# Kernel optimization log

Hardware: AMD Instinct MI355X
Metric: run time of the kernel (lower is better)

The kernel has to match this reference:

```python
import jax, jax.numpy as jnp
import numpy as np

B, N, IN_DIM, D, H, L = 4, 2048, 1, 256, 8, 4
DH = D // H          # 32 head dim
ROPE_D = DH // 2     # 16 = rotary dim per spatial axis (relative_emb_dim=2)
MIN_FREQ_SCALE = 64.0  # scale / min_freq = 1.0 / (1/64)
EPS = 1e-5


def setup_inputs():
    key = jax.random.key(0)
    ks = jax.random.split(key, 12)
    s = 0.02
    return {
        'h': jax.random.normal(ks[0], (B, N, IN_DIM), jnp.float32),
        'pos': jax.random.uniform(ks[1], (B, N, 2), jnp.float32),
        'proj_w': jax.random.normal(ks[2], (IN_DIM, D), jnp.float32) * s,
        'proj_b': jnp.zeros((D,), jnp.float32),
        'qkv_w': jax.random.normal(ks[3], (L, D, 3 * D), jnp.float32) * s,
        'out_w': jax.random.normal(ks[4], (L, D, D), jnp.float32) * s,
        'out_b': jnp.zeros((L, D), jnp.float32),
        'O_w': jax.random.normal(ks[5], (L, D, D), jnp.float32) * s,
        'O_b': jnp.zeros((L, D), jnp.float32),
        'ffn1_w': jax.random.normal(ks[6], (L, D, 2 * D), jnp.float32) * s,
        'ffn1_b': jnp.zeros((L, 2 * D), jnp.float32),
        'ffn2_w': jax.random.normal(ks[7], (L, 2 * D, D), jnp.float32) * s,
        'ffn2_b': jnp.zeros((L, D), jnp.float32),
        'ln1_g': jnp.ones((L, D), jnp.float32),
        'ln1_b': jnp.zeros((L, D), jnp.float32),
        'ln2_g': jnp.ones((L, D), jnp.float32),
        'ln2_b': jnp.zeros((L, D), jnp.float32),
        'final_w': jax.random.normal(ks[8], (D, D), jnp.float32) * s,
    }


def _rope_freqs(coords):
    # coords: (B, N) -> freqs (B, N, ROPE_D)
    inv_freq = 1.0 / (10000.0 ** (jnp.arange(0, ROPE_D, 2, dtype=jnp.float32) / ROPE_D))
    f = (coords * MIN_FREQ_SCALE)[..., None] * inv_freq
    return jnp.concatenate([f, f], axis=-1)


def _rotate_half(x):
    d = x.shape[-1] // 2
    return jnp.concatenate([-x[..., d:], x[..., :d]], axis=-1)


def _apply_rope(t, f):
    return t * jnp.cos(f) + _rotate_half(t) * jnp.sin(f)


def _apply_2d_rope(t, ft, fx):
    d = t.shape[-1] // 2
    return jnp.concatenate([_apply_rope(t[..., :d], ft), _apply_rope(t[..., d:], fx)], axis=-1)


def _ln(x, g, b):
    m = jnp.mean(x, -1, keepdims=True)
    v = jnp.mean((x - m) ** 2, -1, keepdims=True)
    return (x - m) / jnp.sqrt(v + EPS) * g + b


def _forward(h, pos, proj_w, proj_b, qkv_w, out_w, out_b, O_w, O_b,
             ffn1_w, ffn1_b, ffn2_w, ffn2_b, ln1_g, ln1_b, ln2_g, ln2_b, final_w):
    h = h @ proj_w + proj_b                      # (B, N, D)
    ft = _rope_freqs(pos[..., 0])[:, None]       # (B, 1, N, ROPE_D) broadcast over heads
    fx = _rope_freqs(pos[..., 1])[:, None]
    scale = DH ** -0.5
    for l in range(L):
        qkv = h @ qkv_w[l]                       # (B, N, 3D)
        q, k, v = jnp.split(qkv, 3, axis=-1)
        to_heads = lambda t: t.reshape(B, N, H, DH).transpose(0, 2, 1, 3)
        q, k, v = to_heads(q), to_heads(k), to_heads(v)
        q = _apply_2d_rope(q, ft, fx)
        k = _apply_2d_rope(k, ft, fx)
        attn = jax.nn.softmax(jnp.einsum('bhid,bhjd->bhij', q, k) * scale, axis=-1)
        o = jnp.einsum('bhij,bhjd->bhid', attn, v)
        o = o.transpose(0, 2, 1, 3).reshape(B, N, D)
        o = o @ out_w[l] + out_b[l]              # attention to_out
        o = o @ O_w[l] + O_b[l]                  # layer O projection
        h = _ln(h + o, ln1_g[l], ln1_b[l])
        f = jax.nn.relu(h @ ffn1_w[l] + ffn1_b[l]) @ ffn2_w[l] + ffn2_b[l]
        h = _ln(h + f, ln2_g[l], ln2_b[l])
    return h @ final_w


def reference(h, pos, proj_w, proj_b, qkv_w, out_w, out_b, O_w, O_b,
              ffn1_w, ffn1_b, ffn2_w, ffn2_b, ln1_g, ln1_b, ln2_g, ln2_b, final_w):
    return _forward(h, pos, proj_w, proj_b, qkv_w, out_w, out_b, O_w, O_b,
                    ffn1_w, ffn1_b, ffn2_w, ffn2_b, ln1_g, ln1_b, ln2_g, ln2_b, final_w)
```

## Files before the change

kernel.cpp:

```cpp
#include <hip/hip_runtime.h>
#include <math.h>

#define B_ 4
#define N_ 2048
#define D_ 256
#define H_ 8
#define L_ 4
#define DH_ 32

typedef float f32x4 __attribute__((ext_vector_type(4)));
typedef short short8 __attribute__((ext_vector_type(8)));
typedef unsigned short ushort_t;
typedef ushort_t ushortx4 __attribute__((ext_vector_type(4)));
typedef ushort_t ushortx8 __attribute__((ext_vector_type(8)));

static __device__ __forceinline__ ushort_t f2bf(float x) {
    unsigned int u = __float_as_uint(x);
    unsigned int r = (u + 0x7fffu + ((u >> 16) & 1u)) >> 16;
    return (ushort_t)r;
}

static __device__ __forceinline__ unsigned int cvt_pk_bf16(float a, float b) {
    unsigned int w;
    asm("v_cvt_pk_bf16_f32 %0, %1, %2" : "=v"(w) : "v"(a), "v"(b));
    return w;
}

__global__ __launch_bounds__(256) void proj_kernel(
    const float* __restrict__ hin, const float* __restrict__ w,
    const float* __restrict__ bias, float* __restrict__ hout,
    ushort_t* __restrict__ hb)
{
    long idx = (long)blockIdx.x * 256 + threadIdx.x;
    long bn = idx >> 6;
    int d4 = (int)(idx & 63) << 2;
    float hv = hin[bn];
    float4 wv = *(const float4*)&w[d4];
    float4 bv = *(const float4*)&bias[d4];
    float4 o;
    o.x = hv * wv.x + bv.x;
    o.y = hv * wv.y + bv.y;
    o.z = hv * wv.z + bv.z;
    o.w = hv * wv.w + bv.w;
    *(float4*)&hout[bn * D_ + d4] = o;
    ushortx4 ob;
    ob[0] = f2bf(o.x); ob[1] = f2bf(o.y); ob[2] = f2bf(o.z); ob[3] = f2bf(o.w);
    *(ushortx4*)&hb[bn * D_ + d4] = ob;
}

__global__ __launch_bounds__(256) void rope_table_kernel(
    const float* __restrict__ pos, float* __restrict__ tab)
{
    int i = blockIdx.x * 256 + threadIdx.x;
    if (i >= B_ * N_) return;
    float t = pos[i * 2 + 0] * 64.0f;
    float x = pos[i * 2 + 1] * 64.0f;
    float* o = tab + (long)i * 32;
    const float log2_1e4_over8 = 13.28771237954945f / 8.0f;
    #pragma unroll
    for (int j = 0; j < 8; ++j) {
        float invf = exp2f(-(float)j * log2_1e4_over8);
        float st, ct, sx, cx;
        sincosf(t * invf, &st, &ct);
        sincosf(x * invf, &sx, &cx);
        o[j]      = ct;
        o[8 + j]  = st;
        o[16 + j] = cx;
        o[24 + j] = sx;
    }
}

__global__ __launch_bounds__(256) void rope_convert_kernel(
    const float* __restrict__ qkv, const float* __restrict__ tab,
    ushort_t* __restrict__ Qb, ushort_t* __restrict__ Kb)
{
    const float F = 0.17677669529663687f * 1.4426950408889634f;
    long idx = (long)blockIdx.x * 256 + threadIdx.x;
    int p = (int)(idx & 15);
    int h = (int)((idx >> 4) & 7);
    long bn = idx >> 7;
    int half = p >> 3;
    int j = p & 7;
    const float* tb = tab + bn * 32;
    float c = tb[half * 16 + j];
    float s = tb[half * 16 + 8 + j];
    float cF = c * F, sF = s * F;
    int b = (int)(bn >> 11);
    int n = (int)(bn & 2047);
    long obase = ((long)(b * H_ + h) * N_ + n) * DH_;
    const float* base = qkv + bn * (3 * D_) + h * DH_ + half * 16 + j;
    int d0 = half * 16 + j;
    float q0 = base[0], q1 = base[8];
    Qb[obase + d0]     = f2bf(q0 * cF - q1 * sF);
    Qb[obase + d0 + 8] = f2bf(q1 * cF + q0 * sF);
    float k0 = base[D_], k1 = base[D_ + 8];
    Kb[obase + d0]     = f2bf(k0 * c - k1 * s);
    Kb[obase + d0 + 8] = f2bf(k1 * c + k0 * s);
}

__global__ __launch_bounds__(256) void vtrans_kernel(
    const float* __restrict__ qkv, ushort_t* __restrict__ Vt)
{
    int bh = blockIdx.y;
    int b = bh >> 3, h = bh & 7;
    int n0 = blockIdx.x << 6;
    __shared__ float T[64][36];
    int t = threadIdx.x;
    int r = t >> 2, c0 = (t & 3) << 3;
    const float* src = qkv + ((long)b * N_ + n0 + r) * (3 * D_) + 2 * D_ + h * DH_ + c0;
    float4 a = ((const float4*)src)[0];
    float4 bb = ((const float4*)src)[1];
    *(float4*)&T[r][c0] = a;
    *(float4*)&T[r][c0 + 4] = bb;
    __syncthreads();
    int d = t >> 3, n8 = (t & 7) << 3;
    ushortx8 o;
    #pragma unroll
    for (int i = 0; i < 8; ++i) o[i] = f2bf(T[n8 + i][d]);
    *(ushortx8*)&Vt[((long)bh * DH_ + d) * N_ + n0 + n8] = o;
}

__global__ __launch_bounds__(256) void wprep_kernel(
    const float* __restrict__ qkv_w, const float* __restrict__ out_w,
    const float* __restrict__ O_w, const float* __restrict__ ffn1_w,
    const float* __restrict__ ffn2_w, const float* __restrict__ final_w,
    ushort_t* __restrict__ WT)
{
    int bid = blockIdx.x;
    const float* src; ushort_t* dst; int K, Nn, tile;
    if (bid < 192)      { int l = bid / 48;        tile = bid % 48;        src = qkv_w  + (long)l * 196608; dst = WT + (long)l * 196608;           K = 256; Nn = 768; }
    else if (bid < 256) { int r = bid - 192; int l = r / 16; tile = r % 16; src = out_w  + (long)l * 65536;  dst = WT + 786432  + (long)l * 65536;  K = 256; Nn = 256; }
    else if (bid < 320) { int r = bid - 256; int l = r / 16; tile = r % 16; src = O_w    + (long)l * 65536;  dst = WT + 1048576 + (long)l * 65536;  K = 256; Nn = 256; }
    else if (bid < 448) { int r = bid - 320; int l = r / 32; tile = r % 32; src = ffn1_w + (long)l * 131072; dst = WT + 1310720 + (long)l * 131072; K = 256; Nn = 512; }
    else if (bid < 576) { int r = bid - 448; int l = r / 32; tile = r % 32; src = ffn2_w + (long)l * 131072; dst = WT + 1835008 + (long)l * 131072; K = 512; Nn = 256; }
    else                { tile = bid - 576;                                 src = final_w;                   dst = WT + 2359296;                    K = 256; Nn = 256; }
    int ntn = Nn >> 6;
    int kt = (tile / ntn) << 6;
    int nt = (tile % ntn) << 6;
    __shared__ float Tl[64][65];
    int t = threadIdx.x;
    int kr = t >> 2, nc0 = (t & 3) << 4;
    const float* sp = src + (long)(kt + kr) * Nn + nt + nc0;
    float4 v0 = ((const float4*)sp)[0];
    float4 v1 = ((const float4*)sp)[1];
    float4 v2 = ((const float4*)sp)[2];
    float4 v3 = ((const float4*)sp)[3];
    float* tr = &Tl[kr][nc0];
    tr[0] = v0.x; tr[1] = v0.y; tr[2] = v0.z; tr[3] = v0.w;
    tr[4] = v1.x; tr[5] = v1.y; tr[6] = v1.z; tr[7] = v1.w;
    tr[8] = v2.x; tr[9] = v2.y; tr[10] = v2.z; tr[11] = v2.w;
    tr[12] = v3.x; tr[13] = v3.y; tr[14] = v3.z; tr[15] = v3.w;
    __syncthreads();
    int n = t >> 2, kc0 = (t & 3) << 4;
    ushortx8 o0, o1;
    #pragma unroll
    for (int i = 0; i < 8; ++i) o0[i] = f2bf(Tl[kc0 + i][n]);
    #pragma unroll
    for (int i = 0; i < 8; ++i) o1[i] = f2bf(Tl[kc0 + 8 + i][n]);
    ushort_t* dp = dst + (long)(nt + n) * K + kt + kc0;
    *(ushortx8*)dp = o0;
    *(ushortx8*)(dp + 8) = o1;
}

__global__ __launch_bounds__(256) void gemm_mfma(
    const ushort_t* __restrict__ A, const ushort_t* __restrict__ BT,
    const float* __restrict__ bias, void* __restrict__ Cout,
    int N, int K, int flags)
{
    __shared__ ushort_t sA[64 * 64];
    __shared__ ushort_t sB[64 * 64];
    int tid = threadIdx.x;
    int wid = tid >> 6, lane = tid & 63;
    int lo = lane & 15, hi = lane >> 4;
    int wm = wid >> 1, wn = wid & 1;
    int m0 = blockIdx.y << 6, n0 = blockIdx.x << 6;

    int srow = tid >> 3;
    int sslot = tid & 7;
    const ushort_t* Ap  = A  + (long)(m0 + srow) * K + sslot * 8;
    const ushort_t* Ap2 = Ap + 32 * (long)K;
    const ushort_t* Bp  = BT + (long)(n0 + srow) * K + sslot * 8;
    const ushort_t* Bp2 = Bp + 32 * (long)K;
    int wa1 = srow * 64 + (sslot ^ (srow & 7)) * 8;
    int wa2 = (srow + 32) * 64 + (sslot ^ (srow & 7)) * 8;

    f32x4 acc[2][2];
    #pragma unroll
    for (int i = 0; i < 2; ++i)
        #pragma unroll
        for (int j = 0; j < 2; ++j) acc[i][j] = (f32x4){0.f, 0.f, 0.f, 0.f};

    int ar0 = (wm * 32 + lo) * 64;
    int ar1 = (wm * 32 + 16 + lo) * 64;
    int br0 = (wn * 32 + lo) * 64;
    int br1 = (wn * 32 + 16 + lo) * 64;
    int swz = lo & 7;

    for (int kt = 0; kt < K; kt += 64) {
        ushortx8 a1 = *(const ushortx8*)(Ap + kt);
        ushortx8 a2 = *(const ushortx8*)(Ap2 + kt);
        ushortx8 b1 = *(const ushortx8*)(Bp + kt);
        ushortx8 b2 = *(const ushortx8*)(Bp2 + kt);
        __syncthreads();
        *(ushortx8*)&sA[wa1] = a1;
        *(ushortx8*)&sA[wa2] = a2;
        *(ushortx8*)&sB[wa1] = b1;
        *(ushortx8*)&sB[wa2] = b2;
        __syncthreads();
        #pragma unroll
        for (int kf = 0; kf < 2; ++kf) {
            int ks = ((kf * 4 + hi) ^ swz) * 8;
            short8 a0 = *(const short8*)&sA[ar0 + ks];
            short8 a1f = *(const short8*)&sA[ar1 + ks];
            short8 b0 = *(const short8*)&sB[br0 + ks];
            short8 b1f = *(const short8*)&sB[br1 + ks];
            acc[0][0] = __builtin_amdgcn_mfma_f32_16x16x32_bf16(a0, b0, acc[0][0], 0, 0, 0);
            acc[0][1] = __builtin_amdgcn_mfma_f32_16x16x32_bf16(a0, b1f, acc[0][1], 0, 0, 0);
            acc[1][0] = __builtin_amdgcn_mfma_f32_16x16x32_bf16(a1f, b0, acc[1][0], 0, 0, 0);
            acc[1][1] = __builtin_amdgcn_mfma_f32_16x16x32_bf16(a1f, b1f, acc[1][1], 0, 0, 0);
        }
    }

    #pragma unroll
    for (int nf = 0; nf < 2; ++nf) {
        int col = n0 + wn * 32 + nf * 16 + lo;
        float bv = (flags & 1) ? bias[col] : 0.f;
        #pragma unroll
        for (int mf = 0; mf < 2; ++mf) {
            #pragma unroll
            for (int j = 0; j < 4; ++j) {
                float v = acc[mf][nf][j] + bv;
                if (flags & 2) v = fmaxf(v, 0.f);
                long row = m0 + wm * 32 + mf * 16 + hi * 4 + j;
                if (flags & 4) ((ushort_t*)Cout)[row * N + col] = f2bf(v);
                else           ((float*)Cout)[row * N + col] = v;
            }
        }
    }
}

__global__ __launch_bounds__(256) void attn_mfma2(
    const ushort_t* __restrict__ Qb, const ushort_t* __restrict__ Kb,
    const ushort_t* __restrict__ Vt, ushort_t* __restrict__ o)
{
    int bh = blockIdx.y;
    int tid = threadIdx.x;
    int wid = tid >> 6, lane = tid & 63;
    int lo = lane & 15, hi = lane >> 4;
    int q0 = (blockIdx.x << 6) + wid * 16;

    __shared__ ushort_t Vl[2][32][136];
    __shared__ ushort_t Pl[4][16][136];

    const ushort_t* Qbase = Qb + (long)bh * N_ * DH_;
    const ushort_t* Kbase = Kb + (long)bh * N_ * DH_;
    const ushort_t* Vbase = Vt + (long)bh * DH_ * N_;

    short8 qf = *(const short8*)&Qbase[(long)(q0 + lo) * DH_ + hi * 8];

    int vrow = tid >> 4;
    int vc8 = (tid & 15) << 3;

    {
        short8 v0 = *(const short8*)&Vbase[(long)vrow * N_ + vc8];
        short8 v1 = *(const short8*)&Vbase[(long)(vrow + 16) * N_ + vc8];
        *(short8*)&Vl[0][vrow][vc8] = v0;
        *(short8*)&Vl[0][vrow + 16][vc8] = v1;
    }
    __syncthreads();

    float m = -1e30f, l = 0.f;
    f32x4 acc0 = {0.f, 0.f, 0.f, 0.f}, acc1 = {0.f, 0.f, 0.f, 0.f};

    for (int it = 0; it < N_ / 128; ++it) {
        int k0 = it << 7;
        int buf = it & 1;
        short8 nv0, nv1;
        if (it < N_ / 128 - 1) {
            nv0 = *(const short8*)&Vbase[(long)vrow * N_ + k0 + 128 + vc8];
            nv1 = *(const short8*)&Vbase[(long)(vrow + 16) * N_ + k0 + 128 + vc8];
        }
        f32x4 s[8];
        const f32x4 zz = {0.f, 0.f, 0.f, 0.f};
        #pragma unroll
        for (int t = 0; t < 8; ++t) {
            short8 kf = *(const short8*)&Kbase[(long)(k0 + 16 * t + lo) * DH_ + hi * 8];
            s[t] = __builtin_amdgcn_mfma_f32_16x16x32_bf16(kf, qf, zz, 0, 0, 0);
        }
        f32x4 m4 = s[0];
        #pragma unroll
        for (int t = 1; t < 8; ++t) {
            m4[0] = fmaxf(m4[0], s[t][0]); m4[1] = fmaxf(m4[1], s[t][1]);
            m4[2] = fmaxf(m4[2], s[t][2]); m4[3] = fmaxf(m4[3], s[t][3]);
        }
        float pmax = fmaxf(fmaxf(m4[0], m4[1]), fmaxf(m4[2], m4[3]));
        pmax = fmaxf(pmax, __shfl_xor(pmax, 16, 64));
        pmax = fmaxf(pmax, __shfl_xor(pmax, 32, 64));
        if (!__all(pmax <= m + 8.f)) {
            float mn = fmaxf(m, pmax);
            float corr = __builtin_amdgcn_exp2f(m - mn);
            m = mn;
            l *= corr;
            acc0 *= corr;
            acc1 *= corr;
        }
        #pragma unroll
        for (int t = 0; t < 8; ++t) {
            s[t][0] = __builtin_amdgcn_exp2f(s[t][0] - m);
            s[t][1] = __builtin_amdgcn_exp2f(s[t][1] - m);
            s[t][2] = __builtin_amdgcn_exp2f(s[t][2] - m);
            s[t][3] = __builtin_amdgcn_exp2f(s[t][3] - m);
        }
        f32x4 sv = s[0];
        #pragma unroll
        for (int t = 1; t < 8; ++t) sv += s[t];
        float sum = (sv[0] + sv[1]) + (sv[2] + sv[3]);
        sum += __shfl_xor(sum, 16, 64);
        sum += __shfl_xor(sum, 32, 64);
        l += sum;
        {
            unsigned int* Pw = (unsigned int*)&Pl[wid][lo][0];
            #pragma unroll
            for (int t = 0; t < 8; ++t) {
                Pw[8 * t + 2 * hi]     = cvt_pk_bf16(s[t][0], s[t][1]);
                Pw[8 * t + 2 * hi + 1] = cvt_pk_bf16(s[t][2], s[t][3]);
            }
        }
        if (it < N_ / 128 - 1) {
            *(short8*)&Vl[buf ^ 1][vrow][vc8] = nv0;
            *(short8*)&Vl[buf ^ 1][vrow + 16][vc8] = nv1;
        }
        #pragma unroll
        for (int c = 0; c < 4; ++c) {
            short8 pa  = *(const short8*)&Pl[wid][lo][32 * c + 8 * hi];
            short8 vb0 = *(const short8*)&Vl[buf][lo][32 * c + 8 * hi];
            short8 vb1 = *(const short8*)&Vl[buf][16 + lo][32 * c + 8 * hi];
            acc0 = __builtin_amdgcn_mfma_f32_16x16x32_bf16(pa, vb0, acc0, 0, 0, 0);
            acc1 = __builtin_amdgcn_mfma_f32_16x16x32_bf16(pa, vb1, acc1, 0, 0, 0);
        }
        __syncthreads();
    }

    float invl = 1.f / l;
    int b = bh >> 3, h = bh & 7;
    #pragma unroll
    for (int j = 0; j < 4; ++j) {
        float iv = __shfl(invl, 4 * hi + j, 64);
        long row = (long)b * N_ + q0 + 4 * hi + j;
        o[row * D_ + h * DH_ + lo]      = f2bf(acc0[j] * iv);
        o[row * D_ + h * DH_ + 16 + lo] = f2bf(acc1[j] * iv);
    }
}

__global__ __launch_bounds__(256) void add_ln_kernel(
    float* __restrict__ h, const float* __restrict__ r,
    const float* __restrict__ g, const float* __restrict__ be,
    ushort_t* __restrict__ hb)
{
    int row = blockIdx.x * 4 + (threadIdx.x >> 6);
    int lane = threadIdx.x & 63;
    long off = (long)row * D_ + (lane << 2);
    float4 x = *(float4*)&h[off];
    float4 rr = *(const float4*)&r[off];
    x.x += rr.x; x.y += rr.y; x.z += rr.z; x.w += rr.w;
    float s = x.x + x.y + x.z + x.w;
    #pragma unroll
    for (int k = 1; k < 64; k <<= 1) s += __shfl_xor(s, k, 64);
    float mean = s * (1.f / 256.f);
    float dx = x.x - mean, dy = x.y - mean, dz = x.z - mean, dw = x.w - mean;
    float sq = dx * dx + dy * dy + dz * dz + dw * dw;
    #pragma unroll
    for (int k = 1; k < 64; k <<= 1) sq += __shfl_xor(sq, k, 64);
    float rstd = rsqrtf(sq * (1.f / 256.f) + 1e-5f);
    float4 gv = *(const float4*)&g[lane << 2];
    float4 bv = *(const float4*)&be[lane << 2];
    float4 o;
    o.x = dx * rstd * gv.x + bv.x;
    o.y = dy * rstd * gv.y + bv.y;
    o.z = dz * rstd * gv.z + bv.z;
    o.w = dw * rstd * gv.w + bv.w;
    *(float4*)&h[off] = o;
    ushortx4 ob;
    ob[0] = f2bf(o.x); ob[1] = f2bf(o.y); ob[2] = f2bf(o.z); ob[3] = f2bf(o.w);
    *(ushortx4*)&hb[off] = ob;
}

extern "C" void kernel_launch(void* const* d_in, const int* in_sizes, int n_in,
                              void* d_out, int out_size, void* d_ws, size_t ws_size,
                              hipStream_t stream) {
    const float* h_in    = (const float*)d_in[0];
    const float* pos     = (const float*)d_in[1];
    const float* proj_w  = (const float*)d_in[2];
    const float* proj_b  = (const float*)d_in[3];
    const float* qkv_w   = (const float*)d_in[4];
    const float* out_w   = (const float*)d_in[5];
    const float* out_b   = (const float*)d_in[6];
    const float* O_w     = (const float*)d_in[7];
    const float* O_b     = (const float*)d_in[8];
    const float* ffn1_w  = (const float*)d_in[9];
    const float* ffn1_b  = (const float*)d_in[10];
    const float* ffn2_w  = (const float*)d_in[11];
    const float* ffn2_b  = (const float*)d_in[12];
    const float* ln1_g   = (const float*)d_in[13];
    const float* ln1_b   = (const float*)d_in[14];
    const float* ln2_g   = (const float*)d_in[15];
    const float* ln2_b   = (const float*)d_in[16];
    const float* final_w = (const float*)d_in[17];
    float* out = (float*)d_out;

    float* ws   = (float*)d_ws;
    float* h    = ws;
    float* hb_f = h + 2097152;
    float* tab  = hb_f + 1048576;
    float* WT_f = tab + 262144;
    float* R    = WT_f + 1212416;
    float* QKV  = R + 6291456;
    float* tf   = QKV + 3145728;

    ushort_t* hb  = (ushort_t*)hb_f;
    ushort_t* WT  = (ushort_t*)WT_f;
    float*    qkvf = R;
    ushort_t* aob = (ushort_t*)R;
    ushort_t* t1b = (ushort_t*)(R + 1048576);
    ushort_t* fb  = (ushort_t*)(R + 2097152);
    ushort_t* Qb  = (ushort_t*)QKV;
    ushort_t* Kb  = Qb + 2097152;
    ushort_t* Vtg = Kb + 2097152;

    const long qkvT_off  = 0;
    const long outT_off  = 786432;
    const long OT_off    = 1048576;
    const long ffn1T_off = 1310720;
    const long ffn2T_off = 1835008;
    const long finT_off  = 2359296;

    const long M = (long)B_ * N_;

    wprep_kernel<<<592, 256, 0, stream>>>(qkv_w, out_w, O_w, ffn1_w, ffn2_w, final_w, WT);
    proj_kernel<<<(M * 64) / 256, 256, 0, stream>>>(h_in, proj_w, proj_b, h, hb);
    rope_table_kernel<<<(B_ * N_) / 256, 256, 0, stream>>>(pos, tab);

    for (int l = 0; l < L_; ++l) {
        gemm_mfma<<<dim3(768 / 64, M / 64), 256, 0, stream>>>(
            hb, WT + qkvT_off + (long)l * 196608, nullptr, qkvf, 768, 256, 0);
        rope_convert_kernel<<<(M * H_ * 16) / 256, 256, 0, stream>>>(qkvf, tab, Qb, Kb);
        vtrans_kernel<<<dim3(N_ / 64, B_ * H_), 256, 0, stream>>>(qkvf, Vtg);
        attn_mfma2<<<dim3(N_ / 64, B_ * H_), 256, 0, stream>>>(Qb, Kb, Vtg, aob);
        gemm_mfma<<<dim3(256 / 64, M / 64), 256, 0, stream>>>(
            aob, WT + outT_off + (long)l * 65536, out_b + (long)l * D_, t1b, 256, 256, 1 | 4);
        gemm_mfma<<<dim3(256 / 64, M / 64), 256, 0, stream>>>(
            t1b, WT + OT_off + (long)l * 65536, O_b + (long)l * D_, tf, 256, 256, 1);
        add_ln_kernel<<<M / 4, 256, 0, stream>>>(
            h, tf, ln1_g + (long)l * D_, ln1_b + (long)l * D_, hb);
        gemm_mfma<<<dim3(512 / 64, M / 64), 256, 0, stream>>>(
            hb, WT + ffn1T_off + (long)l * 131072, ffn1_b + (long)l * 2 * D_, fb, 512, 256, 1 | 2 | 4);
        gemm_mfma<<<dim3(256 / 64, M / 64), 256, 0, stream>>>(
            fb, WT + ffn2T_off + (long)l * 131072, ffn2_b + (long)l * D_, tf, 256, 512, 1);
        add_ln_kernel<<<M / 4, 256, 0, stream>>>(
            h, tf, ln2_g + (long)l * D_, ln2_b + (long)l * D_, hb);
    }
    gemm_mfma<<<dim3(256 / 64, M / 64), 256, 0, stream>>>(
        hb, WT + finT_off, nullptr, out, 256, 256, 0);
}
```

Before: 565.3 us.

## Fold out/O projections, pipeline GEMM via LDS DMA, register-resident 32x32 attention

Precomputes the product of the attention output weight and the layer O weight (and the folded bias) once per call, so each layer runs one projection GEMM instead of two. Replaces the GEMM with a 128x64 tile version that double-buffers operands through direct global-to-LDS loads with explicit waitcnt and barriers. Rewrites attention to use 32x32x16 MFMAs with P kept in registers via permlane32 swaps instead of LDS, with K/V prefetched into registers. Risks include bf16 rounding of the folded weights, fewer blocks for small GEMMs, and more register pressure in attention.

```diff
diff --git a/kernel.cpp b/kernel.cpp
--- a/kernel.cpp
+++ b/kernel.cpp
@@ -9,10 +9,14 @@
 #define DH_ 32
 
 typedef float f32x4 __attribute__((ext_vector_type(4)));
+typedef float f32x16 __attribute__((ext_vector_type(16)));
 typedef short short8 __attribute__((ext_vector_type(8)));
 typedef unsigned short ushort_t;
 typedef ushort_t ushortx4 __attribute__((ext_vector_type(4)));
 typedef ushort_t ushortx8 __attribute__((ext_vector_type(8)));
+
+typedef __attribute__((address_space(3))) unsigned int lds_u32_t;
+typedef __attribute__((address_space(1))) unsigned int glb_u32_t;
 
 static __device__ __forceinline__ ushort_t f2bf(float x) {
     unsigned int u = __float_as_uint(x);
@@ -162,76 +166,178 @@
     *(ushortx8*)(dp + 8) = o1;
 }
 
-__global__ __launch_bounds__(256) void gemm_mfma(
+__global__ __launch_bounds__(256) void wfold_kernel(
+    const float* __restrict__ out_w, const float* __restrict__ O_w,
+    ushort_t* __restrict__ WTp)
+{
+    int l = blockIdx.x >> 4;
+    int t4 = blockIdx.x & 15;
+    int k0 = (t4 >> 2) << 6, n0 = (t4 & 3) << 6;
+    const float* Am = out_w + (long)l * 65536;
+    const float* Bm = O_w + (long)l * 65536;
+    ushort_t* dst = WTp + (long)l * 65536;
+    __shared__ float sA[16][68];
+    __shared__ float sB[16][64];
+    int tid = threadIdx.x;
+    int tx = tid & 15, ty = tid >> 4;
+    int arow = tid >> 2, acol = (tid & 3) << 2;
+    int brow = tid >> 4, bcol = (tid & 15) << 2;
+    const float* Aptr = Am + (long)(k0 + arow) * 256 + acol;
+    const float* Bptr = Bm + (long)brow * 256 + n0 + bcol;
+    float acc[4][4] = {{0.f}};
+    for (int jt = 0; jt < 256; jt += 16) {
+        float4 av = *(const float4*)(Aptr + jt);
+        float4 bv = *(const float4*)(Bptr + (long)jt * 256);
+        __syncthreads();
+        sA[acol + 0][arow] = av.x;
+        sA[acol + 1][arow] = av.y;
+        sA[acol + 2][arow] = av.z;
+        sA[acol + 3][arow] = av.w;
+        *(float4*)&sB[brow][bcol] = bv;
+        __syncthreads();
+        #pragma unroll
+        for (int kk = 0; kk < 16; ++kk) {
+            float4 a = *(const float4*)&sA[kk][ty << 2];
+            float4 b = *(const float4*)&sB[kk][tx << 2];
+            acc[0][0] += a.x * b.x; acc[0][1] += a.x * b.y; acc[0][2] += a.x * b.z; acc[0][3] += a.x * b.w;
+            acc[1][0] += a.y * b.x; acc[1][1] += a.y * b.y; acc[1][2] += a.y * b.z; acc[1][3] += a.y * b.w;
+            acc[2][0] += a.z * b.x; acc[2][1] += a.z * b.y; acc[2][2] += a.z * b.z; acc[2][3] += a.z * b.w;
+            acc[3][0] += a.w * b.x; acc[3][1] += a.w * b.y; acc[3][2] += a.w * b.z; acc[3][3] += a.w * b.w;
+        }
+    }
+    #pragma unroll
+    for (int i = 0; i < 4; ++i) {
+        int k = k0 + (ty << 2) + i;
+        #pragma unroll
+        for (int c = 0; c < 4; ++c) {
+            int n = n0 + (tx << 2) + c;
+            dst[(long)n * 256 + k] = f2bf(acc[i][c]);
+        }
+    }
+}
+
+__global__ __launch_bounds__(256) void bfold_kernel(
+    const float* __restrict__ out_b, const float* __restrict__ O_w,
+    const float* __restrict__ O_b, float* __restrict__ bp)
+{
+    int l = blockIdx.x >> 3;
+    int n = ((blockIdx.x & 7) << 5) + (threadIdx.x & 31);
+    int jg = threadIdx.x >> 5;
+    const float* Bm = O_w + (long)l * 65536;
+    float acc = 0.f;
+    #pragma unroll 8
+    for (int j = jg * 32; j < jg * 32 + 32; ++j)
+        acc += out_b[l * 256 + j] * Bm[(long)j * 256 + n];
+    __shared__ float red[8][32];
+    red[jg][threadIdx.x & 31] = acc;
+    __syncthreads();
+    if (threadIdx.x < 32) {
+        int nn = ((blockIdx.x & 7) << 5) + threadIdx.x;
+        float s = O_b[l * 256 + nn];
+        #pragma unroll
+        for (int g = 0; g < 8; ++g) s += red[g][threadIdx.x];
+        bp[l * 256 + nn] = s;
+    }
+}
+
+__global__ __launch_bounds__(256) void gemm_mfma2(
     const ushort_t* __restrict__ A, const ushort_t* __restrict__ BT,
     const float* __restrict__ bias, void* __restrict__ Cout,
     int N, int K, int flags)
 {
-    __shared__ ushort_t sA[64 * 64];
-    __shared__ ushort_t sB[64 * 64];
+    __shared__ ushort_t sA[2][8192];
+    __shared__ ushort_t sB[2][4096];
     int tid = threadIdx.x;
     int wid = tid >> 6, lane = tid & 63;
     int lo = lane & 15, hi = lane >> 4;
     int wm = wid >> 1, wn = wid & 1;
-    int m0 = blockIdx.y << 6, n0 = blockIdx.x << 6;
-
-    int srow = tid >> 3;
-    int sslot = tid & 7;
-    const ushort_t* Ap  = A  + (long)(m0 + srow) * K + sslot * 8;
-    const ushort_t* Ap2 = Ap + 32 * (long)K;
-    const ushort_t* Bp  = BT + (long)(n0 + srow) * K + sslot * 8;
-    const ushort_t* Bp2 = Bp + 32 * (long)K;
-    int wa1 = srow * 64 + (sslot ^ (srow & 7)) * 8;
-    int wa2 = (srow + 32) * 64 + (sslot ^ (srow & 7)) * 8;
-
-    f32x4 acc[2][2];
-    #pragma unroll
-    for (int i = 0; i < 2; ++i)
+    int m0 = blockIdx.y << 7, n0 = blockIdx.x << 6;
+
+    int lrow = lane >> 3;
+    int slot = lane & 7;
+    const ushort_t* Ag[4];
+    const ushort_t* Bg[2];
+    #pragma unroll
+    for (int c = 0; c < 4; ++c) {
+        int arow = (wid << 5) + (c << 3) + lrow;
+        Ag[c] = A + (long)(m0 + arow) * K + ((slot ^ lrow) << 3);
+    }
+    #pragma unroll
+    for (int c = 0; c < 2; ++c) {
+        int brow = (wid << 4) + (c << 3) + lrow;
+        Bg[c] = BT + (long)(n0 + brow) * K + ((slot ^ lrow) << 3);
+    }
+
+#define STAGE(buf, koff) do { \
+    _Pragma("unroll") \
+    for (int c = 0; c < 4; ++c) \
+        __builtin_amdgcn_global_load_lds((const glb_u32_t*)(Ag[c] + (koff)), \
+            (lds_u32_t*)&sA[buf][((wid << 5) + (c << 3)) << 6], 16, 0, 0); \
+    _Pragma("unroll") \
+    for (int c = 0; c < 2; ++c) \
+        __builtin_amdgcn_global_load_lds((const glb_u32_t*)(Bg[c] + (koff)), \
+            (lds_u32_t*)&sB[buf][((wid << 4) + (c << 3)) << 6], 16, 0, 0); \
+} while (0)
+
+    f32x4 acc[4][2];
+    #pragma unroll
+    for (int i = 0; i < 4; ++i)
         #pragma unroll
         for (int j = 0; j < 2; ++j) acc[i][j] = (f32x4){0.f, 0.f, 0.f, 0.f};
 
-    int ar0 = (wm * 32 + lo) * 64;
-    int ar1 = (wm * 32 + 16 + lo) * 64;
-    int br0 = (wn * 32 + lo) * 64;
-    int br1 = (wn * 32 + 16 + lo) * 64;
+    int ar[4], br[2];
+    #pragma unroll
+    for (int mf = 0; mf < 4; ++mf) ar[mf] = ((wm << 6) + (mf << 4) + lo) << 6;
+    #pragma unroll
+    for (int nf = 0; nf < 2; ++nf) br[nf] = ((wn << 5) + (nf << 4) + lo) << 6;
     int swz = lo & 7;
 
-    for (int kt = 0; kt < K; kt += 64) {
-        ushortx8 a1 = *(const ushortx8*)(Ap + kt);
-        ushortx8 a2 = *(const ushortx8*)(Ap2 + kt);
-        ushortx8 b1 = *(const ushortx8*)(Bp + kt);
-        ushortx8 b2 = *(const ushortx8*)(Bp2 + kt);
-        __syncthreads();
-        *(ushortx8*)&sA[wa1] = a1;
-        *(ushortx8*)&sA[wa2] = a2;
-        *(ushortx8*)&sB[wa1] = b1;
-        *(ushortx8*)&sB[wa2] = b2;
-        __syncthreads();
+    int nk = K >> 6;
+    STAGE(0, 0);
+    for (int s = 0; s < nk; ++s) {
+        int buf = s & 1;
+        if (s + 1 < nk) {
+            STAGE(buf ^ 1, (s + 1) << 6);
+            asm volatile("s_waitcnt vmcnt(6)" ::: "memory");
+        } else {
+            asm volatile("s_waitcnt vmcnt(0)" ::: "memory");
+        }
+        __builtin_amdgcn_s_barrier();
+        asm volatile("" ::: "memory");
         #pragma unroll
-        for (int kf = 0; kf < 2; ++kf) {
-            int ks = ((kf * 4 + hi) ^ swz) * 8;
-            short8 a0 = *(const short8*)&sA[ar0 + ks];
-            short8 a1f = *(const short8*)&sA[ar1 + ks];
-            short8 b0 = *(const short8*)&sB[br0 + ks];
-            short8 b1f = *(const short8*)&sB[br1 + ks];
+        for (int ks = 0; ks < 2; ++ks) {
+            int ko = (((ks << 2) + hi) ^ swz) << 3;
+            short8 a0 = *(const short8*)&sA[buf][ar[0] + ko];
+            short8 a1 = *(const short8*)&sA[buf][ar[1] + ko];
+            short8 a2 = *(const short8*)&sA[buf][ar[2] + ko];
+            short8 a3 = *(const short8*)&sA[buf][ar[3] + ko];
+            short8 b0 = *(const short8*)&sB[buf][br[0] + ko];
+            short8 b1 = *(const short8*)&sB[buf][br[1] + ko];
             acc[0][0] = __builtin_amdgcn_mfma_f32_16x16x32_bf16(a0, b0, acc[0][0], 0, 0, 0);
-            acc[0][1] = __builtin_amdgcn_mfma_f32_16x16x32_bf16(a0, b1f, acc[0][1], 0, 0, 0);
-            acc[1][0] = __builtin_amdgcn_mfma_f32_16x16x32_bf16(a1f, b0, acc[1][0], 0, 0, 0);
-            acc[1][1] = __builtin_amdgcn_mfma_f32_16x16x32_bf16(a1f, b1f, acc[1][1], 0, 0, 0);
+            acc[0][1] = __builtin_amdgcn_mfma_f32_16x16x32_bf16(a0, b1, acc[0][1], 0, 0, 0);
+            acc[1][0] = __builtin_amdgcn_mfma_f32_16x16x32_bf16(a1, b0, acc[1][0], 0, 0, 0);
+            acc[1][1] = __builtin_amdgcn_mfma_f32_16x16x32_bf16(a1, b1, acc[1][1], 0, 0, 0);
+            acc[2][0] = __builtin_amdgcn_mfma_f32_16x16x32_bf16(a2, b0, acc[2][0], 0, 0, 0);
+            acc[2][1] = __builtin_amdgcn_mfma_f32_16x16x32_bf16(a2, b1, acc[2][1], 0, 0, 0);
+            acc[3][0] = __builtin_amdgcn_mfma_f32_16x16x32_bf16(a3, b0, acc[3][0], 0, 0, 0);
+            acc[3][1] = __builtin_amdgcn_mfma_f32_16x16x32_bf16(a3, b1, acc[3][1], 0, 0, 0);
         }
-    }
+        asm volatile("" ::: "memory");
+        __builtin_amdgcn_s_barrier();
+    }
+#undef STAGE
 
     #pragma unroll
     for (int nf = 0; nf < 2; ++nf) {
-        int col = n0 + wn * 32 + nf * 16 + lo;
+        int col = n0 + (wn << 5) + (nf << 4) + lo;
         float bv = (flags & 1) ? bias[col] : 0.f;
         #pragma unroll
-        for (int mf = 0; mf < 2; ++mf) {
+        for (int mf = 0; mf < 4; ++mf) {
             #pragma unroll
             for (int j = 0; j < 4; ++j) {
                 float v = acc[mf][nf][j] + bv;
                 if (flags & 2) v = fmaxf(v, 0.f);
-                long row = m0 + wm * 32 + mf * 16 + hi * 4 + j;
+                long row = m0 + (wm << 6) + (mf << 4) + (hi << 2) + j;
                 if (flags & 4) ((ushort_t*)Cout)[row * N + col] = f2bf(v);
                 else           ((float*)Cout)[row * N + col] = v;
             }
@@ -239,116 +345,120 @@
     }
 }
 
-__global__ __launch_bounds__(256) void attn_mfma2(
+__global__ __launch_bounds__(256) void attn_mfma4(
     const ushort_t* __restrict__ Qb, const ushort_t* __restrict__ Kb,
     const ushort_t* __restrict__ Vt, ushort_t* __restrict__ o)
 {
     int bh = blockIdx.y;
     int tid = threadIdx.x;
     int wid = tid >> 6, lane = tid & 63;
-    int lo = lane & 15, hi = lane >> 4;
-    int q0 = (blockIdx.x << 6) + wid * 16;
-
-    __shared__ ushort_t Vl[2][32][136];
-    __shared__ ushort_t Pl[4][16][136];
-
-    const ushort_t* Qbase = Qb + (long)bh * N_ * DH_;
-    const ushort_t* Kbase = Kb + (long)bh * N_ * DH_;
-    const ushort_t* Vbase = Vt + (long)bh * DH_ * N_;
-
-    short8 qf = *(const short8*)&Qbase[(long)(q0 + lo) * DH_ + hi * 8];
-
-    int vrow = tid >> 4;
-    int vc8 = (tid & 15) << 3;
-
-    {
-        short8 v0 = *(const short8*)&Vbase[(long)vrow * N_ + vc8];
-        short8 v1 = *(const short8*)&Vbase[(long)(vrow + 16) * N_ + vc8];
-        *(short8*)&Vl[0][vrow][vc8] = v0;
-        *(short8*)&Vl[0][vrow + 16][vc8] = v1;
-    }
-    __syncthreads();
-
-    float m = -1e30f, l = 0.f;
-    f32x4 acc0 = {0.f, 0.f, 0.f, 0.f}, acc1 = {0.f, 0.f, 0.f, 0.f};
-
-    for (int it = 0; it < N_ / 128; ++it) {
-        int k0 = it << 7;
-        int buf = it & 1;
-        short8 nv0, nv1;
-        if (it < N_ / 128 - 1) {
-            nv0 = *(const short8*)&Vbase[(long)vrow * N_ + k0 + 128 + vc8];
-            nv1 = *(const short8*)&Vbase[(long)(vrow + 16) * N_ + k0 + 128 + vc8];
-        }
-        f32x4 s[8];
-        const f32x4 zz = {0.f, 0.f, 0.f, 0.f};
-        #pragma unroll
-        for (int t = 0; t < 8; ++t) {
-            short8 kf = *(const short8*)&Kbase[(long)(k0 + 16 * t + lo) * DH_ + hi * 8];
-            s[t] = __builtin_amdgcn_mfma_f32_16x16x32_bf16(kf, qf, zz, 0, 0, 0);
-        }
-        f32x4 m4 = s[0];
-        #pragma unroll
-        for (int t = 1; t < 8; ++t) {
-            m4[0] = fmaxf(m4[0], s[t][0]); m4[1] = fmaxf(m4[1], s[t][1]);
-            m4[2] = fmaxf(m4[2], s[t][2]); m4[3] = fmaxf(m4[3], s[t][3]);
-        }
-        float pmax = fmaxf(fmaxf(m4[0], m4[1]), fmaxf(m4[2], m4[3]));
-        pmax = fmaxf(pmax, __shfl_xor(pmax, 16, 64));
-        pmax = fmaxf(pmax, __shfl_xor(pmax, 32, 64));
-        if (!__all(pmax <= m + 8.f)) {
-            float mn = fmaxf(m, pmax);
-            float corr = __builtin_amdgcn_exp2f(m - mn);
-            m = mn;
-            l *= corr;
-            acc0 *= corr;
-            acc1 *= corr;
-        }
-        #pragma unroll
-        for (int t = 0; t < 8; ++t) {
-            s[t][0] = __builtin_amdgcn_exp2f(s[t][0] - m);
-            s[t][1] = __builtin_amdgcn_exp2f(s[t][1] - m);
-            s[t][2] = __builtin_amdgcn_exp2f(s[t][2] - m);
-            s[t][3] = __builtin_amdgcn_exp2f(s[t][3] - m);
-        }
-        f32x4 sv = s[0];
-        #pragma unroll
-        for (int t = 1; t < 8; ++t) sv += s[t];
-        float sum = (sv[0] + sv[1]) + (sv[2] + sv[3]);
-        sum += __shfl_xor(sum, 16, 64);
-        sum += __shfl_xor(sum, 32, 64);
-        l += sum;
-        {
-            unsigned int* Pw = (unsigned int*)&Pl[wid][lo][0];
-            #pragma unroll
-            for (int t = 0; t < 8; ++t) {
-                Pw[8 * t + 2 * hi]     = cvt_pk_bf16(s[t][0], s[t][1]);
-                Pw[8 * t + 2 * hi + 1] = cvt_pk_bf16(s[t][2], s[t][3]);
-            }
-        }
-        if (it < N_ / 128 - 1) {
-            *(short8*)&Vl[buf ^ 1][vrow][vc8] = nv0;
-            *(short8*)&Vl[buf ^ 1][vrow + 16][vc8] = nv1;
-        }
-        #pragma unroll
-        for (int c = 0; c < 4; ++c) {
-            short8 pa  = *(const short8*)&Pl[wid][lo][32 * c + 8 * hi];
-            short8 vb0 = *(const short8*)&Vl[buf][lo][32 * c + 8 * hi];
-            short8 vb1 = *(const short8*)&Vl[buf][16 + lo][32 * c + 8 * hi];
-            acc0 = __builtin_amdgcn_mfma_f32_16x16x32_bf16(pa, vb0, acc0, 0, 0, 0);
-            acc1 = __builtin_amdgcn_mfma_f32_16x16x32_bf16(pa, vb1, acc1, 0, 0, 0);
-        }
-        __syncthreads();
-    }
-
-    float invl = 1.f / l;
+    int lq = lane & 31;
+    int half = lane >> 5;
+    int qbase = (blockIdx.x << 7) + wid * 32;
+
+    const ushort_t* Qp = Qb + (long)bh * N_ * DH_;
+    const ushort_t* kp = Kb + (long)bh * N_ * DH_ + lq * DH_ + half * 8;
+    const ushort_t* vp = Vt + (long)bh * DH_ * N_ + (long)lq * N_ + half * 8;
+
+    short8 qf0 = *(const short8*)&Qp[(long)(qbase + lq) * DH_ + half * 8];
+    short8 qf1 = *(const short8*)&Qp[(long)(qbase + lq) * DH_ + 16 + half * 8];
+
+    f32x16 acc;
+    #pragma unroll
+    for (int r = 0; r < 16; ++r) acc[r] = 0.f;
+    float m = -1e30f, lsum = 0.f;
+
+    short8 k00 = *(const short8*)(kp +  0 * DH_);
+    short8 k01 = *(const short8*)(kp +  0 * DH_ + 16);
+    short8 k10 = *(const short8*)(kp + 32 * DH_);
+    short8 k11 = *(const short8*)(kp + 32 * DH_ + 16);
+    short8 v00 = *(const short8*)(vp +  0);
+    short8 v01 = *(const short8*)(vp + 16);
+    short8 v10 = *(const short8*)(vp + 32);
+    short8 v11 = *(const short8*)(vp + 48);
+
+#define ATTN_TILE(K00, K01, K10, K11, V00, V01, V10, V11) do {                  \
+    f32x16 sa, sb;                                                              \
+    _Pragma("unroll")                                                           \
+    for (int r = 0; r < 16; ++r) { sa[r] = 0.f; sb[r] = 0.f; }                  \
+    sa = __builtin_amdgcn_mfma_f32_32x32x16_bf16(K00, qf0, sa, 0, 0, 0);        \
+    sa = __builtin_amdgcn_mfma_f32_32x32x16_bf16(K01, qf1, sa, 0, 0, 0);        \
+    sb = __builtin_amdgcn_mfma_f32_32x32x16_bf16(K10, qf0, sb, 0, 0, 0);        \
+    sb = __builtin_amdgcn_mfma_f32_32x32x16_bf16(K11, qf1, sb, 0, 0, 0);        \
+    float pmax = fmaxf(sa[0], sb[0]);                                           \
+    _Pragma("unroll")                                                           \
+    for (int r = 1; r < 16; ++r) pmax = fmaxf(pmax, fmaxf(sa[r], sb[r]));       \
+    pmax = fmaxf(pmax, __shfl_xor(pmax, 32, 64));                               \
+    if (!__all(pmax <= m + 8.f)) {                                              \
+        float mn = fmaxf(m, pmax);                                              \
+        float corr = __builtin_amdgcn_exp2f(m - mn);                            \
+        m = mn; lsum *= corr;                                                   \
+        _Pragma("unroll")                                                       \
+        for (int r = 0; r < 16; ++r) {                                          \
+            int qr = (r & 3) + 8 * (r >> 2) + 4 * half;                         \
+            acc[r] *= __shfl(corr, qr, 64);                                     \
+        }                                                                       \
+    }                                                                           \
+    float sum = 0.f;                                                            \
+    _Pragma("unroll")                                                           \
+    for (int r = 0; r < 16; ++r) {                                              \
+        sa[r] = __builtin_amdgcn_exp2f(sa[r] - m); sum += sa[r];                \
+        sb[r] = __builtin_amdgcn_exp2f(sb[r] - m); sum += sb[r];                \
+    }                                                                           \
+    sum += __shfl_xor(sum, 32, 64);                                             \
+    lsum += sum;                                                                \
+    unsigned int a0 = cvt_pk_bf16(sa[0], sa[1]),   a1 = cvt_pk_bf16(sa[2], sa[3]);   \
+    unsigned int a2 = cvt_pk_bf16(sa[4], sa[5]),   a3 = cvt_pk_bf16(sa[6], sa[7]);   \
+    unsigned int a4 = cvt_pk_bf16(sa[8], sa[9]),   a5 = cvt_pk_bf16(sa[10], sa[11]); \
+    unsigned int a6 = cvt_pk_bf16(sa[12], sa[13]), a7 = cvt_pk_bf16(sa[14], sa[15]); \
+    unsigned int b0 = cvt_pk_bf16(sb[0], sb[1]),   b1 = cvt_pk_bf16(sb[2], sb[3]);   \
+    unsigned int b2 = cvt_pk_bf16(sb[4], sb[5]),   b3 = cvt_pk_bf16(sb[6], sb[7]);   \
+    unsigned int b4 = cvt_pk_bf16(sb[8], sb[9]),   b5 = cvt_pk_bf16(sb[10], sb[11]); \
+    unsigned int b6 = cvt_pk_bf16(sb[12], sb[13]), b7 = cvt_pk_bf16(sb[14], sb[15]); \
+    asm volatile("v_permlane32_swap_b32 %0, %1" : "+v"(a0), "+v"(a2));          \
+    asm volatile("v_permlane32_swap_b32 %0, %1" : "+v"(a1), "+v"(a3));          \
+    asm volatile("v_permlane32_swap_b32 %0, %1" : "+v"(a4), "+v"(a6));          \
+    asm volatile("v_permlane32_swap_b32 %0, %1" : "+v"(a5), "+v"(a7));          \
+    asm volatile("v_permlane32_swap_b32 %0, %1" : "+v"(b0), "+v"(b2));          \
+    asm volatile("v_permlane32_swap_b32 %0, %1" : "+v"(b1), "+v"(b3));          \
+    asm volatile("v_permlane32_swap_b32 %0, %1" : "+v"(b4), "+v"(b6));          \
+    asm volatile("v_permlane32_swap_b32 %0, %1" : "+v"(b5), "+v"(b7));          \
+    union { unsigned int u[4]; short8 s8; } p0, p1, p2, p3;                     \
+    p0.u[0] = a0; p0.u[1] = a1; p0.u[2] = a2; p0.u[3] = a3;                     \
+    p1.u[0] = a4; p1.u[1] = a5; p1.u[2] = a6; p1.u[3] = a7;                     \
+    p2.u[0] = b0; p2.u[1] = b1; p2.u[2] = b2; p2.u[3] = b3;                     \
+    p3.u[0] = b4; p3.u[1] = b5; p3.u[2] = b6; p3.u[3] = b7;                     \
+    acc = __builtin_amdgcn_mfma_f32_32x32x16_bf16(p0.s8, V00, acc, 0, 0, 0);    \
+    acc = __builtin_amdgcn_mfma_f32_32x32x16_bf16(p1.s8, V01, acc, 0, 0, 0);    \
+    acc = __builtin_amdgcn_mfma_f32_32x32x16_bf16(p2.s8, V10, acc, 0, 0, 0);    \
+    acc = __builtin_amdgcn_mfma_f32_32x32x16_bf16(p3.s8, V11, acc, 0, 0, 0);    \
+} while (0)
+
+    for (int it = 0; it < N_ / 64 - 1; ++it) {
+        long kn = (long)(it + 1) << 6;
+        short8 nk00 = *(const short8*)(kp + (kn +  0) * DH_);
+        short8 nk01 = *(const short8*)(kp + (kn +  0) * DH_ + 16);
+        short8 nk10 = *(const short8*)(kp + (kn + 32) * DH_);
+        short8 nk11 = *(const short8*)(kp + (kn + 32) * DH_ + 16);
+        short8 nv00 = *(const short8*)(vp + kn);
+        short8 nv01 = *(const short8*)(vp + kn + 16);
+        short8 nv10 = *(const short8*)(vp + kn + 32);
+        short8 nv11 = *(const short8*)(vp + kn + 48);
+        ATTN_TILE(k00, k01, k10, k11, v00, v01, v10, v11);
+        k00 = nk00; k01 = nk01; k10 = nk10; k11 = nk11;
+        v00 = nv00; v01 = nv01; v10 = nv10; v11 = nv11;
+    }
+    ATTN_TILE(k00, k01, k10, k11, v00, v01, v10, v11);
+#undef ATTN_TILE
+
+    float invl = 1.f / lsum;
     int b = bh >> 3, h = bh & 7;
     #pragma unroll
-    for (int j = 0; j < 4; ++j) {
-        float iv = __shfl(invl, 4 * hi + j, 64);
-        long row = (long)b * N_ + q0 + 4 * hi + j;
-        o[row * D_ + h * DH_ + lo]      = f2bf(acc0[j] * iv);
-        o[row * D_ + h * DH_ + 16 + lo] = f2bf(acc1[j] * iv);
+    for (int r = 0; r < 16; ++r) {
+        int qr = (r & 3) + 8 * (r >> 2) + 4 * half;
+        float iv = __shfl(invl, qr, 64);
+        long row = (long)b * N_ + qbase + qr;
+        o[row * D_ + h * DH_ + lq] = f2bf(acc[r] * iv);
     }
 }
 
@@ -421,15 +531,15 @@
     ushort_t* WT  = (ushort_t*)WT_f;
     float*    qkvf = R;
     ushort_t* aob = (ushort_t*)R;
-    ushort_t* t1b = (ushort_t*)(R + 1048576);
     ushort_t* fb  = (ushort_t*)(R + 2097152);
+    float*    tf32 = R + 4194304;
     ushort_t* Qb  = (ushort_t*)QKV;
     ushort_t* Kb  = Qb + 2097152;
     ushort_t* Vtg = Kb + 2097152;
+    ushort_t* WTp = (ushort_t*)tf;
+    float*    bp  = tf + 131072;
 
     const long qkvT_off  = 0;
-    const long outT_off  = 786432;
-    const long OT_off    = 1048576;
     const long ffn1T_off = 1310720;
     const long ffn2T_off = 1835008;
     const long finT_off  = 2359296;
@@ -437,28 +547,28 @@
     const long M = (long)B_ * N_;
 
     wprep_kernel<<<592, 256, 0, stream>>>(qkv_w, out_w, O_w, ffn1_w, ffn2_w, final_w, WT);
+    wfold_kernel<<<64, 256, 0, stream>>>(out_w, O_w, WTp);
+    bfold_kernel<<<32, 256, 0, stream>>>(out_b, O_w, O_b, bp);
     proj_kernel<<<(M * 64) / 256, 256, 0, stream>>>(h_in, proj_w, proj_b, h, hb);
     rope_table_kernel<<<(B_ * N_) / 256, 256, 0, stream>>>(pos, tab);
 
     for (int l = 0; l < L_; ++l) {
-        gemm_mfma<<<dim3(768 / 64, M / 64), 256, 0, stream>>>(
+        gemm_mfma2<<<dim3(768 / 64, M / 128), 256, 0, stream>>>(
             hb, WT + qkvT_off + (long)l * 196608, nullptr, qkvf, 768, 256, 0);
         rope_convert_kernel<<<(M * H_ * 16) / 256, 256, 0, stream>>>(qkvf, tab, Qb, Kb);
         vtrans_kernel<<<dim3(N_ / 64, B_ * H_), 256, 0, stream>>>(qkvf, Vtg);
-        attn_mfma2<<<dim3(N_ / 64, B_ * H_), 256, 0, stream>>>(Qb, Kb, Vtg, aob);
-        gemm_mfma<<<dim3(256 / 64, M / 64), 256, 0, stream>>>(
-            aob, WT + outT_off + (long)l * 65536, out_b + (long)l * D_, t1b, 256, 256, 1 | 4);
-        gemm_mfma<<<dim3(256 / 64, M / 64), 256, 0, stream>>>(
-            t1b, WT + OT_off + (long)l * 65536, O_b + (long)l * D_, tf, 256, 256, 1);
+        attn_mfma4<<<dim3(N_ / 128, B_ * H_), 256, 0, stream>>>(Qb, Kb, Vtg, aob);
+        gemm_mfma2<<<dim3(256 / 64, M / 128), 256, 0, stream>>>(
+            aob, WTp + (long)l * 65536, bp + (long)l * 256, tf32, 256, 256, 1);
         add_ln_kernel<<<M / 4, 256, 0, stream>>>(
-            h, tf, ln1_g + (long)l * D_, ln1_b + (long)l * D_, hb);
-        gemm_mfma<<<dim3(512 / 64, M / 64), 256, 0, stream>>>(
+            h, tf32, ln1_g + (long)l * D_, ln1_b + (long)l * D_, hb);
+        gemm_mfma2<<<dim3(512 / 64, M / 128), 256, 0, stream>>>(
             hb, WT + ffn1T_off + (long)l * 131072, ffn1_b + (long)l * 2 * D_, fb, 512, 256, 1 | 2 | 4);
-        gemm_mfma<<<dim3(256 / 64, M / 64), 256, 0, stream>>>(
-            fb, WT + ffn2T_off + (long)l * 131072, ffn2_b + (long)l * D_, tf, 256, 512, 1);
+        gemm_mfma2<<<dim3(256 / 64, M / 128), 256, 0, stream>>>(
+            fb, WT + ffn2T_off + (long)l * 131072, ffn2_b + (long)l * D_, tf32, 256, 512, 1);
         add_ln_kernel<<<M / 4, 256, 0, stream>>>(
-            h, tf, ln2_g + (long)l * D_, ln2_b + (long)l * D_, hb);
-    }
-    gemm_mfma<<<dim3(256 / 64, M / 64), 256, 0, stream>>>(
+            h, tf32, ln2_g + (long)l * D_, ln2_b + (long)l * D_, hb);
+    }
+    gemm_mfma2<<<dim3(256 / 64, M / 128), 256, 0, stream>>>(
         hb, WT + finT_off, nullptr, out, 256, 256, 0);
 }
```

Result: no change. 559.6 us (-1.0%).
